# Performance work log

Hardware: AMD Instinct MI355X
Metric: run time of the kernel (lower is better)

## Reference

```python
import jax, jax.numpy as jnp
import numpy as np

V, E, H, T = 100000, 256, 256, 8192


def setup_inputs() -> dict:
    key = jax.random.key(0)
    k0, k1, k2, k3, k4, k5 = jax.random.split(key, 6)
    s = 1.0 / np.sqrt(H)  # PyTorch LSTM init bound
    tokens = jax.random.randint(k0, (T,), 0, V)
    embedding = jax.random.normal(k1, (V, E), jnp.float32) * 0.02
    W_ih = jax.random.uniform(k2, (4 * H, E), jnp.float32, -s, s)
    W_hh = jax.random.uniform(k3, (4 * H, H), jnp.float32, -s, s)
    b_ih = jax.random.uniform(k4, (4 * H,), jnp.float32, -s, s)
    b_hh = jax.random.uniform(k5, (4 * H,), jnp.float32, -s, s)
    return {"tokens": tokens, "embedding": embedding, "W_ih": W_ih,
            "W_hh": W_hh, "b_ih": b_ih, "b_hh": b_hh}


def reference(tokens, embedding, W_ih, W_hh, b_ih, b_hh):
    # Flattened tree traversal: one embed + one LSTM cell step per token,
    # hidden state threaded through, all per-token hiddens collected.
    emb = embedding[tokens]                      # [T, E] gather (memory-bound)
    # precompute input contribution for every step (batched GEMM)
    xg = emb @ W_ih.T + (b_ih + b_hh)            # [T, 4H]

    def step(carry, xg_t):
        h, c = carry
        g = xg_t + W_hh @ h                      # [4H]
        i, f, gg, o = jnp.split(g, 4)
        i = jax.nn.sigmoid(i)
        f = jax.nn.sigmoid(f)
        gg = jnp.tanh(gg)
        o = jax.nn.sigmoid(o)
        c = f * c + i * gg
        h = o * jnp.tanh(c)
        return (h, c), h

    h0 = jnp.zeros((H,), emb.dtype)
    c0 = jnp.zeros((H,), emb.dtype)
    (h_last, c_last), hiddens = jax.lax.scan(step, (h0, c0), xg)
    return hiddens, h_last, c_last
```

## Files before the change

### kernel.cpp

```cpp
#include <hip/hip_runtime.h>

#define T_STEPS 8192
#define HID 256
#define NBLK 128
#define THREADS 256
#define SPIN_MAX 4096

#define MAGIC_READY 0x13579BDFu
#define EMPTY_XCD   0xFFFFFFFFu

__device__ __forceinline__ float tanh_fast(float x) { return 2.0f / (1.0f + __expf(-2.0f * x)) - 1.0f; }

__device__ __forceinline__ void st_u64_sc0(unsigned long long* p, unsigned long long v) {
    asm volatile("global_store_dwordx2 %0, %1, off sc0" :: "v"(p), "v"(v) : "memory");
}
__device__ __forceinline__ void ld4_u64_sc0(const unsigned long long* p,
                                            unsigned long long& a, unsigned long long& b,
                                            unsigned long long& c, unsigned long long& d) {
    asm volatile(
        "global_load_dwordx2 %0, %4, off sc0\n\t"
        "global_load_dwordx2 %1, %4, off offset:8 sc0\n\t"
        "global_load_dwordx2 %2, %4, off offset:16 sc0\n\t"
        "global_load_dwordx2 %3, %4, off offset:24 sc0\n\t"
        "s_waitcnt vmcnt(0)"
        : "=&v"(a), "=&v"(b), "=&v"(c), "=&v"(d)
        : "v"(p) : "memory");
}

__global__ __launch_bounds__(THREADS, 1)
void lstm_scan(const int* __restrict__ tokens,
               const float* __restrict__ emb,
               const float* __restrict__ Wih,
               const float* __restrict__ Whh,
               const float* __restrict__ bih,
               const float* __restrict__ bhh,
               float* __restrict__ out,
               unsigned long long* __restrict__ hbL,
               unsigned long long* __restrict__ hbA,
               unsigned* __restrict__ ctl)
{
    __shared__ int s_role;
    if (threadIdx.x == 0) {
        unsigned xcc;
        asm volatile("s_getreg_b32 %0, hwreg(HW_REG_XCC_ID, 0, 4)" : "=s"(xcc));
        unsigned* ready   = ctl + 0;
        unsigned* elected = ctl + 1;
        unsigned* cnt     = ctl + 2;
        if (blockIdx.x == 0) {
            for (int i = 0; i < 8; ++i)
                __hip_atomic_store(cnt + i, 0u, __ATOMIC_RELAXED, __HIP_MEMORY_SCOPE_AGENT);
            __hip_atomic_store(elected, EMPTY_XCD, __ATOMIC_RELAXED, __HIP_MEMORY_SCOPE_AGENT);
            __hip_atomic_store(ready, MAGIC_READY, __ATOMIC_RELEASE, __HIP_MEMORY_SCOPE_AGENT);
        }
        while (__hip_atomic_load(ready, __ATOMIC_ACQUIRE, __HIP_MEMORY_SCOPE_AGENT) != MAGIC_READY)
            asm volatile("s_sleep 1");
        unsigned r = __hip_atomic_fetch_add(cnt + xcc, 1u, __ATOMIC_RELAXED, __HIP_MEMORY_SCOPE_AGENT);
        if (r == 15u) {
            unsigned expv = EMPTY_XCD;
            __hip_atomic_compare_exchange_strong(elected, &expv, xcc,
                __ATOMIC_RELAXED, __ATOMIC_RELAXED, __HIP_MEMORY_SCOPE_AGENT);
        }
        unsigned e;
        while ((e = __hip_atomic_load(elected, __ATOMIC_ACQUIRE, __HIP_MEMORY_SCOPE_AGENT)) == EMPTY_XCD)
            asm volatile("s_sleep 1");
        s_role = (xcc == e && r < 16u) ? (int)r : -1;
    }
    __syncthreads();
    const int w = s_role;
    if (w < 0) return;

    const int tid  = threadIdx.x;
    const int lane = tid & 63;
    const int wave = tid >> 6;
    const int rl   = lane >> 2;
    const int kq   = lane & 3;
    const int r_wg = wave * 16 + rl;
    const int unit_local = r_wg >> 2;
    const int gate = r_wg & 3;
    const int unit = w * 16 + unit_local;
    const int grow = gate * 256 + unit;
    const int kbase = kq * 64;

    float whh[64], wih[64];
    {
        const float* p = Whh + (size_t)grow * 256 + kbase;
        #pragma unroll
        for (int j = 0; j < 64; j += 4) {
            float4 q = *(const float4*)(p + j);
            whh[j] = q.x; whh[j+1] = q.y; whh[j+2] = q.z; whh[j+3] = q.w;
        }
        p = Wih + (size_t)grow * 256 + kbase;
        #pragma unroll
        for (int j = 0; j < 64; j += 4) {
            float4 q = *(const float4*)(p + j);
            wih[j] = q.x; wih[j+1] = q.y; wih[j+2] = q.z; wih[j+3] = q.w;
        }
    }
    const float bias = bih[grow] + bhh[grow];
    const bool owner = ((lane & 15) == 0);
    const float act_scale = (gate == 2) ? 2.0f : 1.0f;
    const float act_off   = (gate == 2) ? 1.0f : 0.0f;

    __shared__ float4 lds_h4[4][17];
    __shared__ float4 lds_e4[2][4][17];

    if (owner) {
        st_u64_sc0(hbL + unit, 0ull);
        __hip_atomic_store(hbA + unit, 0ull, __ATOMIC_RELAXED, __HIP_MEMORY_SCOPE_AGENT);
    }
    if (wave == 1) {
        int tk = tokens[0];
        float4 e = *(const float4*)(emb + (size_t)tk * 256 + lane * 4);
        lds_e4[0][lane >> 4][lane & 15] = e;
    }
    float c = 0.0f;
    bool useL2 = true;
    __syncthreads();

    for (int t = 0; t < T_STEPS; ++t) {
        if (wave == 1) {
            int tk = tokens[(t + 1 < T_STEPS) ? t + 1 : t];
            float4 e = *(const float4*)(emb + (size_t)tk * 256 + lane * 4);
            lds_e4[(t + 1) & 1][lane >> 4][lane & 15] = e;
        }
        float acc = 0.0f;
        {
            const float4* eb = lds_e4[t & 1][kq];
            #pragma unroll
            for (int i = 0; i < 16; ++i) {
                float4 v = eb[i];
                acc = fmaf(wih[4*i+0], v.x, acc);
                acc = fmaf(wih[4*i+1], v.y, acc);
                acc = fmaf(wih[4*i+2], v.z, acc);
                acc = fmaf(wih[4*i+3], v.w, acc);
            }
        }
        if (wave == 0) {
            const size_t po = (size_t)(t & 1) * 256 + lane * 4;
            unsigned long long p0, p1, p2, p3;
            const unsigned int tt = (unsigned int)t;
            bool got = false;
            if (useL2) {
                const unsigned long long* hb = hbL + po;
                int n = 0;
                for (;;) {
                    ld4_u64_sc0(hb, p0, p1, p2, p3);
                    if (((unsigned int)(p0 >> 32) == tt) & ((unsigned int)(p1 >> 32) == tt) &
                        ((unsigned int)(p2 >> 32) == tt) & ((unsigned int)(p3 >> 32) == tt)) {
                        got = true; break;
                    }
                    if (++n > SPIN_MAX) { useL2 = false; break; }
                }
            }
            if (!got) {
                const unsigned long long* hb = hbA + po;
                for (;;) {
                    p0 = __hip_atomic_load(hb + 0, __ATOMIC_RELAXED, __HIP_MEMORY_SCOPE_AGENT);
                    p1 = __hip_atomic_load(hb + 1, __ATOMIC_RELAXED, __HIP_MEMORY_SCOPE_AGENT);
                    p2 = __hip_atomic_load(hb + 2, __ATOMIC_RELAXED, __HIP_MEMORY_SCOPE_AGENT);
                    p3 = __hip_atomic_load(hb + 3, __ATOMIC_RELAXED, __HIP_MEMORY_SCOPE_AGENT);
                    if (((unsigned int)(p0 >> 32) == tt) & ((unsigned int)(p1 >> 32) == tt) &
                        ((unsigned int)(p2 >> 32) == tt) & ((unsigned int)(p3 >> 32) == tt))
                        break;
                }
            }
            union { unsigned int i; float f; } a, b, cc, d;
            a.i = (unsigned int)p0; b.i = (unsigned int)p1;
            cc.i = (unsigned int)p2; d.i = (unsigned int)p3;
            lds_h4[lane >> 4][lane & 15] = make_float4(a.f, b.f, cc.f, d.f);
        }
        __syncthreads();
        {
            const float4* hb4 = lds_h4[kq];
            #pragma unroll
            for (int i = 0; i < 16; ++i) {
                float4 v = hb4[i];
                acc = fmaf(whh[4*i+0], v.x, acc);
                acc = fmaf(whh[4*i+1], v.y, acc);
                acc = fmaf(whh[4*i+2], v.z, acc);
                acc = fmaf(whh[4*i+3], v.w, acc);
            }
        }
        acc += __shfl_xor(acc, 1, 64);
        acc += __shfl_xor(acc, 2, 64);
        acc += bias;
        float ex = __expf(-act_scale * acc);
        float av = act_scale / (1.0f + ex) - act_off;
        const int base = lane & 48;
        float fv = __shfl(av, base + 4,  64);
        float gv = __shfl(av, base + 8,  64);
        float ov = __shfl(av, base + 12, 64);
        if (owner) {
            c = fmaf(fv, c, av * gv);
            float h = ov * tanh_fast(c);
            union { unsigned int i; float f; } u; u.f = h;
            unsigned long long pk =
                (((unsigned long long)(unsigned int)(t + 1)) << 32) | (unsigned long long)u.i;
            const size_t so = (size_t)((t + 1) & 1) * 256 + unit;
            st_u64_sc0(hbL + so, pk);
            __hip_atomic_store(hbA + so, pk, __ATOMIC_RELAXED,
                               __HIP_MEMORY_SCOPE_AGENT);
            out[(size_t)t * HID + unit] = h;
            if (t == T_STEPS - 1) {
                out[(size_t)T_STEPS * HID + unit]       = h;
                out[(size_t)T_STEPS * HID + HID + unit] = c;
            }
        }
    }

    if (w == 0 && tid == 0)
        __hip_atomic_store(ctl + 0, 0u, __ATOMIC_RELAXED, __HIP_MEMORY_SCOPE_AGENT);
}

extern "C" void kernel_launch(void* const* d_in, const int* in_sizes, int n_in,
                              void* d_out, int out_size, void* d_ws, size_t ws_size,
                              hipStream_t stream) {
    const int*   tokens = (const int*)d_in[0];
    const float* emb    = (const float*)d_in[1];
    const float* Wih    = (const float*)d_in[2];
    const float* Whh    = (const float*)d_in[3];
    const float* bih    = (const float*)d_in[4];
    const float* bhh    = (const float*)d_in[5];
    float* out = (float*)d_out;
    unsigned long long* hbL = (unsigned long long*)d_ws;
    unsigned long long* hbA = (unsigned long long*)((char*)d_ws + 4096);
    unsigned* ctl = (unsigned*)((char*)d_ws + 8192);

    lstm_scan<<<NBLK, THREADS, 0, stream>>>(tokens, emb, Wih, Whh, bih, bhh, out, hbL, hbA, ctl);
}
```

Measured before the change: 12.59 ms.

## Keep non-elected blocks spinning on FMA work and split dot-product accumulators

Blocks not elected to run the recurrence no longer exit. They now run a dummy FMA loop until the worker group sets a done flag, apparently to keep the GPU busy or clocks high during the serial scan. Separately, the input and recurrent dot products now use four independent accumulators instead of one chain, which shortens the FMA dependency chain on the per-step critical path. The busy-spinning blocks burn power and could contend for resources, and reassociating the sums slightly changes floating-point rounding.

```diff
diff --git a/kernel.cpp b/kernel.cpp
--- a/kernel.cpp
+++ b/kernel.cpp
@@ -8,6 +8,7 @@
 
 #define MAGIC_READY 0x13579BDFu
 #define EMPTY_XCD   0xFFFFFFFFu
+#define DONE_MAGIC  0x600DD00Eu
 
 __device__ __forceinline__ float tanh_fast(float x) { return 2.0f / (1.0f + __expf(-2.0f * x)) - 1.0f; }
 
@@ -50,6 +51,7 @@
             for (int i = 0; i < 8; ++i)
                 __hip_atomic_store(cnt + i, 0u, __ATOMIC_RELAXED, __HIP_MEMORY_SCOPE_AGENT);
             __hip_atomic_store(elected, EMPTY_XCD, __ATOMIC_RELAXED, __HIP_MEMORY_SCOPE_AGENT);
+            __hip_atomic_store(ctl + 10, 0u, __ATOMIC_RELAXED, __HIP_MEMORY_SCOPE_AGENT);
             __hip_atomic_store(ready, MAGIC_READY, __ATOMIC_RELEASE, __HIP_MEMORY_SCOPE_AGENT);
         }
         while (__hip_atomic_load(ready, __ATOMIC_ACQUIRE, __HIP_MEMORY_SCOPE_AGENT) != MAGIC_READY)
@@ -67,7 +69,23 @@
     }
     __syncthreads();
     const int w = s_role;
-    if (w < 0) return;
+
+    if (w < 0) {
+        float x0 = 1.0f, x1 = 2.0f, x2 = 3.0f, x3 = 4.0f;
+        const float a = 1.0000001f, b = 1e-7f;
+        const unsigned* done = ctl + 10;
+        for (;;) {
+            #pragma unroll 64
+            for (int i = 0; i < 512; ++i) {
+                x0 = fmaf(x0, a, b); x1 = fmaf(x1, a, b);
+                x2 = fmaf(x2, a, b); x3 = fmaf(x3, a, b);
+            }
+            if (__hip_atomic_load(done, __ATOMIC_RELAXED, __HIP_MEMORY_SCOPE_AGENT) == DONE_MAGIC)
+                break;
+        }
+        asm volatile("" :: "v"(x0 + x1 + x2 + x3));
+        return;
+    }
 
     const int tid  = threadIdx.x;
     const int lane = tid & 63;
@@ -123,16 +141,20 @@
             float4 e = *(const float4*)(emb + (size_t)tk * 256 + lane * 4);
             lds_e4[(t + 1) & 1][lane >> 4][lane & 15] = e;
         }
-        float acc = 0.0f;
+        float aA = 0.0f, aB = 0.0f, aC = 0.0f, aD = 0.0f;
         {
             const float4* eb = lds_e4[t & 1][kq];
             #pragma unroll
-            for (int i = 0; i < 16; ++i) {
-                float4 v = eb[i];
-                acc = fmaf(wih[4*i+0], v.x, acc);
-                acc = fmaf(wih[4*i+1], v.y, acc);
-                acc = fmaf(wih[4*i+2], v.z, acc);
-                acc = fmaf(wih[4*i+3], v.w, acc);
+            for (int i = 0; i < 16; i += 4) {
+                float4 v0 = eb[i], v1 = eb[i+1], v2 = eb[i+2], v3 = eb[i+3];
+                aA = fmaf(wih[4*i+ 0], v0.x, aA); aA = fmaf(wih[4*i+ 1], v0.y, aA);
+                aA = fmaf(wih[4*i+ 2], v0.z, aA); aA = fmaf(wih[4*i+ 3], v0.w, aA);
+                aB = fmaf(wih[4*i+ 4], v1.x, aB); aB = fmaf(wih[4*i+ 5], v1.y, aB);
+                aB = fmaf(wih[4*i+ 6], v1.z, aB); aB = fmaf(wih[4*i+ 7], v1.w, aB);
+                aC = fmaf(wih[4*i+ 8], v2.x, aC); aC = fmaf(wih[4*i+ 9], v2.y, aC);
+                aC = fmaf(wih[4*i+10], v2.z, aC); aC = fmaf(wih[4*i+11], v2.w, aC);
+                aD = fmaf(wih[4*i+12], v3.x, aD); aD = fmaf(wih[4*i+13], v3.y, aD);
+                aD = fmaf(wih[4*i+14], v3.z, aD); aD = fmaf(wih[4*i+15], v3.w, aD);
             }
         }
         if (wave == 0) {
@@ -171,16 +193,21 @@
         }
         __syncthreads();
         {
-            const float4* hb4 = lds_h4[kq];
+            const float4* hq = lds_h4[kq];
             #pragma unroll
-            for (int i = 0; i < 16; ++i) {
-                float4 v = hb4[i];
-                acc = fmaf(whh[4*i+0], v.x, acc);
-                acc = fmaf(whh[4*i+1], v.y, acc);
-                acc = fmaf(whh[4*i+2], v.z, acc);
-                acc = fmaf(whh[4*i+3], v.w, acc);
-            }
-        }
+            for (int i = 0; i < 16; i += 4) {
+                float4 v0 = hq[i], v1 = hq[i+1], v2 = hq[i+2], v3 = hq[i+3];
+                aA = fmaf(whh[4*i+ 0], v0.x, aA); aA = fmaf(whh[4*i+ 1], v0.y, aA);
+                aA = fmaf(whh[4*i+ 2], v0.z, aA); aA = fmaf(whh[4*i+ 3], v0.w, aA);
+                aB = fmaf(whh[4*i+ 4], v1.x, aB); aB = fmaf(whh[4*i+ 5], v1.y, aB);
+                aB = fmaf(whh[4*i+ 6], v1.z, aB); aB = fmaf(whh[4*i+ 7], v1.w, aB);
+                aC = fmaf(whh[4*i+ 8], v2.x, aC); aC = fmaf(whh[4*i+ 9], v2.y, aC);
+                aC = fmaf(whh[4*i+10], v2.z, aC); aC = fmaf(whh[4*i+11], v2.w, aC);
+                aD = fmaf(whh[4*i+12], v3.x, aD); aD = fmaf(whh[4*i+13], v3.y, aD);
+                aD = fmaf(whh[4*i+14], v3.z, aD); aD = fmaf(whh[4*i+15], v3.w, aD);
+            }
+        }
+        float acc = (aA + aB) + (aC + aD);
         acc += __shfl_xor(acc, 1, 64);
         acc += __shfl_xor(acc, 2, 64);
         acc += bias;
@@ -208,8 +235,10 @@
         }
     }
 
-    if (w == 0 && tid == 0)
+    if (w == 0 && tid == 0) {
+        __hip_atomic_store(ctl + 10, DONE_MAGIC, __ATOMIC_RELEASE, __HIP_MEMORY_SCOPE_AGENT);
         __hip_atomic_store(ctl + 0, 0u, __ATOMIC_RELAXED, __HIP_MEMORY_SCOPE_AGENT);
+    }
 }
 
 extern "C" void kernel_launch(void* const* d_in, const int* in_sizes, int n_in,
```

After: 12.56 ms. Within noise of the previous version (-0.2%).
